# Performance work log

Measured on AMD Instinct MI355X. Metric: run time of the kernel, lower is better.

Reference implementation:

```python
import jax, jax.numpy as jnp
import numpy as np

IN_FEATURES = 4096
OUT_FEATURES = 4096
CODESZ = 8
CODEBOOK_SIZE = 256


def fwht(x):
    """Normalized fast Walsh-Hadamard transform over the last dim (power of 2).
    Equivalent to x @ (H / sqrt(n)); H symmetric so this serves both
    matmul_hadUt and matmul_hadU in the power-of-2 case (had=None, K=1)."""
    orig_shape = x.shape
    n = orig_shape[-1]
    x = x.reshape(-1, n)
    h = 2
    while h <= n:
        x = x.reshape(-1, n // h, 2, h // 2)
        a, b = x[..., 0, :], x[..., 1, :]
        x = jnp.stack([a + b, a - b], axis=-2)
        h *= 2
    x = x.reshape(orig_shape)
    return x * (1.0 / np.sqrt(n)).astype(np.float32)


def setup_inputs() -> dict:
    key = jax.random.key(0)
    k1, k2, k3, k4, k5, k6 = jax.random.split(key, 6)
    x = jax.random.normal(k1, (4, 2048, IN_FEATURES), dtype=jnp.float32)
    Qidxs = jax.random.randint(k2, (OUT_FEATURES, IN_FEATURES // CODESZ), 0, CODEBOOK_SIZE, dtype=jnp.int32)
    grid = jax.random.normal(k3, (CODEBOOK_SIZE, CODESZ), dtype=jnp.float32)
    SU = jax.random.uniform(k4, (IN_FEATURES,), dtype=jnp.float32)
    SV = jax.random.uniform(k5, (OUT_FEATURES,), dtype=jnp.float32)
    bias = jax.random.normal(k6, (OUT_FEATURES,), dtype=jnp.float32)
    return {"x": x, "Qidxs": Qidxs, "grid": grid, "SU": SU, "SV": SV, "bias": bias}


def reference(x, Qidxs, grid, SU, SV, bias):
    lead = x.shape[:-1]
    h = x.reshape(-1, IN_FEATURES)            # [T, in]
    h = h * SU                                 # scale by SU
    h = fwht(h)                                # matmul_hadUt (input rotation)
    # codebook dequant: gather code vectors and form W_hat [out, in]
    W_hat = grid[Qidxs].reshape(OUT_FEATURES, IN_FEATURES)
    y = h @ W_hat.T                            # [T, out]
    y = fwht(y)[:, :OUT_FEATURES]              # matmul_hadU (output rotation)
    y = y * SV
    y = y.reshape(*lead, OUT_FEATURES) + bias
    return y
```

## Files before the change

### kernel.cpp

```cpp
#include <hip/hip_runtime.h>

#define IN_F 4096
#define OUT_F 4096
#define NROWS 8192
#define BK 32
#define NT (IN_F / BK)

typedef __attribute__((ext_vector_type(4))) float f32x4;
typedef __attribute__((ext_vector_type(8))) short bf16x8;
typedef __attribute__((ext_vector_type(8))) unsigned short u16x8;

__device__ __forceinline__ unsigned short f2bf(float f) {
  union { float f; unsigned u; } x; x.f = f;
  unsigned r = x.u + 0x7FFFu + ((x.u >> 16) & 1u);
  return (unsigned short)(r >> 16);
}

__device__ __forceinline__ void gload_lds16(const unsigned short* g, unsigned short* l) {
  __builtin_amdgcn_global_load_lds((__attribute__((address_space(1))) void*)g,
                                   (__attribute__((address_space(3))) void*)l,
                                   16, 0, 0);
}

__device__ __forceinline__ void bfly16(float v[16]) {
#pragma unroll
  for (int s = 1; s < 16; s <<= 1) {
#pragma unroll
    for (int i = 0; i < 16; ++i) {
      if (!(i & s)) { float a = v[i], b = v[i + s]; v[i] = a + b; v[i + s] = a - b; }
    }
  }
}

__global__ __launch_bounds__(256) void dequant_kernel(const int* __restrict__ Q,
                                                      const float* __restrict__ grid,
                                                      unsigned short* __restrict__ Wb) {
  int g = blockIdx.x * 256 + threadIdx.x;
  int idx = Q[g];
  const f32x4* gp = (const f32x4*)(grid + idx * 8);
  f32x4 v0 = gp[0], v1 = gp[1];
  u16x8 o;
  o[0] = f2bf(v0[0]); o[1] = f2bf(v0[1]); o[2] = f2bf(v0[2]); o[3] = f2bf(v0[3]);
  o[4] = f2bf(v1[0]); o[5] = f2bf(v1[1]); o[6] = f2bf(v1[2]); o[7] = f2bf(v1[3]);
  *(u16x8*)(Wb + (size_t)g * 8) = o;
}

__global__ __launch_bounds__(256) void fwht1_kernel(const float* __restrict__ x,
                                                    const float* __restrict__ SU,
                                                    unsigned short* __restrict__ Hb) {
  __shared__ float buf[4096];
  int tid = threadIdx.x;
  size_t rbase = (size_t)blockIdx.x * IN_F;
  const f32x4* x4 = (const f32x4*)(x + rbase);
  const f32x4* su4 = (const f32x4*)SU;
  f32x4* b4 = (f32x4*)buf;
#pragma unroll
  for (int s = 0; s < 4; ++s) {
    int c = tid + 256 * s;
    f32x4 v = x4[c];
    f32x4 u = su4[c];
    v.x *= u.x; v.y *= u.y; v.z *= u.z; v.w *= u.w;
    b4[c] = v;
  }
  __syncthreads();
  float v[16];
  {
#pragma unroll
    for (int j = 0; j < 4; ++j) {
      f32x4 t4 = b4[tid * 4 + j];
      v[j*4+0] = t4.x; v[j*4+1] = t4.y; v[j*4+2] = t4.z; v[j*4+3] = t4.w;
    }
    bfly16(v);
#pragma unroll
    for (int j = 0; j < 4; ++j) {
      f32x4 t4; t4.x = v[j*4+0]; t4.y = v[j*4+1]; t4.z = v[j*4+2]; t4.w = v[j*4+3];
      b4[tid * 4 + j] = t4;
    }
  }
  __syncthreads();
  {
    int lo = tid & 15, hi = tid >> 4;
    int base = lo + (hi << 8);
#pragma unroll
    for (int j = 0; j < 16; ++j) v[j] = buf[base + (j << 4)];
    bfly16(v);
#pragma unroll
    for (int j = 0; j < 16; ++j) buf[base + (j << 4)] = v[j];
  }
  __syncthreads();
  {
#pragma unroll
    for (int j = 0; j < 16; ++j) v[j] = buf[tid + (j << 8)];
    bfly16(v);
#pragma unroll
    for (int j = 0; j < 16; ++j)
      Hb[rbase + tid + (j << 8)] = f2bf(v[j] * 0.015625f);
  }
}

#define MM(i, A, B) acc[i] = __builtin_amdgcn_mfma_f32_16x16x32_bf16(A, B, acc[i], 0, 0, 0)

__global__ __launch_bounds__(512) void gemm256_kernel(const unsigned short* __restrict__ Hb,
                                                      const unsigned short* __restrict__ Wb,
                                                      float* __restrict__ Y) {
  __shared__ unsigned short lds[4][2][256 * BK];
  const int tid = threadIdx.x;
  const int lane = tid & 63;
  const int wid = tid >> 6;
  const int wr = wid >> 2;
  const int wc = wid & 3;
  const int lrow = lane & 15;
  const int kgrp = lane >> 4;

  const int bid = blockIdx.x;
  const int swz = (bid & 7) * 64 + (bid >> 3);
  const int brow = (swz >> 4) << 8;
  const int bcol = (swz & 15) << 8;

  const unsigned short* Ab = Hb + (size_t)brow * IN_F;
  const unsigned short* Bb = Wb + (size_t)bcol * IN_F;

  const int r0 = tid >> 2;
  const int sc = ((tid & 3) ^ (r0 & 3)) << 3;
  const unsigned short* Ag0 = Ab + (size_t)r0 * IN_F + sc;
  const unsigned short* Ag1 = Ab + (size_t)(r0 + 128) * IN_F + sc;
  const unsigned short* Bg0 = Bb + (size_t)r0 * IN_F + sc;
  const unsigned short* Bg1 = Bb + (size_t)(r0 + 128) * IN_F + sc;

#define STAGE_A(t, s) { gload_lds16(Ag0 + (t) * BK, &lds[s][0][tid * 8]); \
                        gload_lds16(Ag1 + (t) * BK, &lds[s][0][(tid + 512) * 8]); }
#define STAGE_B(t, s) { gload_lds16(Bg0 + (t) * BK, &lds[s][1][tid * 8]); \
                        gload_lds16(Bg1 + (t) * BK, &lds[s][1][(tid + 512) * 8]); }

  auto fragLd = [&](const unsigned short* base, int R) -> bf16x8 {
    return *(const bf16x8*)(base + R * BK + ((kgrp ^ (R & 3)) << 3));
  };

  f32x4 acc[32] = {};

  STAGE_A(0, 0); STAGE_B(0, 0);
  STAGE_A(1, 1); STAGE_B(1, 1);
  STAGE_A(2, 2); STAGE_B(2, 2);
  asm volatile("s_waitcnt vmcnt(8)" ::: "memory");
  asm volatile("s_barrier" ::: "memory");

  for (int t = 0; t < NT; ++t) {
    const int s = t & 3;
    const unsigned short* As = &lds[s][0][0];
    const unsigned short* Bs = &lds[s][1][0];
    bf16x8 a0, a1, a2, a3, b0, b1, b2, b3;

    a0 = fragLd(As, wr * 128 +  0 + lrow);
    a1 = fragLd(As, wr * 128 + 16 + lrow);
    a2 = fragLd(As, wr * 128 + 32 + lrow);
    a3 = fragLd(As, wr * 128 + 48 + lrow);
    b0 = fragLd(Bs, wc * 64 +  0 + lrow);
    b1 = fragLd(Bs, wc * 64 + 16 + lrow);
    b2 = fragLd(Bs, wc * 64 + 32 + lrow);
    b3 = fragLd(Bs, wc * 64 + 48 + lrow);
    if (t + 3 < NT) STAGE_A(t + 3, (t + 3) & 3);
    asm volatile("s_barrier" ::: "memory");
    __builtin_amdgcn_s_setprio(1);
    MM( 0, a0, b0); MM( 1, a0, b1); MM( 2, a0, b2); MM( 3, a0, b3);
    MM( 4, a1, b0); MM( 5, a1, b1); MM( 6, a1, b2); MM( 7, a1, b3);
    MM( 8, a2, b0); MM( 9, a2, b1); MM(10, a2, b2); MM(11, a2, b3);
    MM(12, a3, b0); MM(13, a3, b1); MM(14, a3, b2); MM(15, a3, b3);
    __builtin_amdgcn_s_setprio(0);
    asm volatile("s_barrier" ::: "memory");

    a0 = fragLd(As, wr * 128 +  64 + lrow);
    a1 = fragLd(As, wr * 128 +  80 + lrow);
    a2 = fragLd(As, wr * 128 +  96 + lrow);
    a3 = fragLd(As, wr * 128 + 112 + lrow);
    if (t + 3 < NT) STAGE_B(t + 3, (t + 3) & 3);
    asm volatile("s_barrier" ::: "memory");
    __builtin_amdgcn_s_setprio(1);
    MM(16, a0, b0); MM(17, a0, b1); MM(18, a0, b2); MM(19, a0, b3);
    MM(20, a1, b0); MM(21, a1, b1); MM(22, a1, b2); MM(23, a1, b3);
    MM(24, a2, b0); MM(25, a2, b1); MM(26, a2, b2); MM(27, a2, b3);
    MM(28, a3, b0); MM(29, a3, b1); MM(30, a3, b2); MM(31, a3, b3);
    __builtin_amdgcn_s_setprio(0);
    if (t < NT - 3)       { asm volatile("s_waitcnt vmcnt(8)" ::: "memory"); }
    else if (t == NT - 3) { asm volatile("s_waitcnt vmcnt(4)" ::: "memory"); }
    else if (t == NT - 2) { asm volatile("s_waitcnt vmcnt(0)" ::: "memory"); }
    asm volatile("s_barrier" ::: "memory");
  }

#pragma unroll
  for (int mf = 0; mf < 8; ++mf) {
    int grow = brow + wr * 128 + mf * 16 + kgrp * 4;
    float* yp = Y + (size_t)grow * OUT_F + bcol + wc * 64 + lrow;
#pragma unroll
    for (int r = 0; r < 4; ++r)
#pragma unroll
      for (int n = 0; n < 4; ++n)
        yp[(size_t)r * OUT_F + n * 16] = acc[mf * 4 + n][r];
  }
#undef STAGE_A
#undef STAGE_B
}

__global__ __launch_bounds__(256) void fwht2_kernel(float* __restrict__ Y,
                                                    const float* __restrict__ SV,
                                                    const float* __restrict__ bias) {
  __shared__ float buf[4096];
  int tid = threadIdx.x;
  size_t rbase = (size_t)blockIdx.x * OUT_F;
  f32x4* y4 = (f32x4*)(Y + rbase);
  f32x4* b4 = (f32x4*)buf;
#pragma unroll
  for (int s = 0; s < 4; ++s) {
    int c = tid + 256 * s;
    b4[c] = y4[c];
  }
  __syncthreads();
  float v[16];
  {
#pragma unroll
    for (int j = 0; j < 4; ++j) {
      f32x4 t4 = b4[tid * 4 + j];
      v[j*4+0] = t4.x; v[j*4+1] = t4.y; v[j*4+2] = t4.z; v[j*4+3] = t4.w;
    }
    bfly16(v);
#pragma unroll
    for (int j = 0; j < 4; ++j) {
      f32x4 t4; t4.x = v[j*4+0]; t4.y = v[j*4+1]; t4.z = v[j*4+2]; t4.w = v[j*4+3];
      b4[tid * 4 + j] = t4;
    }
  }
  __syncthreads();
  {
    int lo = tid & 15, hi = tid >> 4;
    int base = lo + (hi << 8);
#pragma unroll
    for (int j = 0; j < 16; ++j) v[j] = buf[base + (j << 4)];
    bfly16(v);
#pragma unroll
    for (int j = 0; j < 16; ++j) buf[base + (j << 4)] = v[j];
  }
  __syncthreads();
  {
#pragma unroll
    for (int j = 0; j < 16; ++j) v[j] = buf[tid + (j << 8)];
    bfly16(v);
#pragma unroll
    for (int j = 0; j < 16; ++j) {
      int col = tid + (j << 8);
      Y[rbase + col] = v[j] * 0.015625f * SV[col] + bias[col];
    }
  }
}

extern "C" void kernel_launch(void* const* d_in, const int* in_sizes, int n_in,
                              void* d_out, int out_size, void* d_ws, size_t ws_size,
                              hipStream_t stream) {
  const float* x     = (const float*)d_in[0];
  const int*   Qidxs = (const int*)d_in[1];
  const float* grid  = (const float*)d_in[2];
  const float* SU    = (const float*)d_in[3];
  const float* SV    = (const float*)d_in[4];
  const float* bias  = (const float*)d_in[5];
  float* out = (float*)d_out;

  unsigned short* Wb = (unsigned short*)d_ws;
  unsigned short* Hb = Wb + (size_t)OUT_F * IN_F;

  hipLaunchKernelGGL(dequant_kernel, dim3((OUT_F * (IN_F / 8)) / 256), dim3(256), 0, stream,
                     Qidxs, grid, Wb);
  hipLaunchKernelGGL(fwht1_kernel, dim3(NROWS), dim3(256), 0, stream, x, SU, Hb);
  hipLaunchKernelGGL(gemm256_kernel, dim3((NROWS / 256) * (OUT_F / 256)), dim3(512), 0, stream,
                     Hb, Wb, out);
  hipLaunchKernelGGL(fwht2_kernel, dim3(NROWS), dim3(256), 0, stream, out, SV, bias);
}
```

Measured before the change: 357.2 us.

## Double-buffer LDS fragment registers and change LDS swizzle in GEMM main loop

Restructures the bf16 GEMM main loop to process two K-tiles per iteration with two register fragment sets, so LDS reads for the next tile are issued while MFMAs for the current tile execute. This cuts barriers from three per tile to about one. Global-to-LDS staging now loads the A and B halves together in one STAGE. The LDS XOR swizzle now keys on (row>>1)&3 instead of row&3, to reduce bank conflicts for the 64-byte row stride. The cost is doubled fragment registers, which may raise VGPR pressure and lower occupancy, plus subtler waitcnt bookkeeping around the 4-slot ring.

```diff
diff --git a/kernel.cpp b/kernel.cpp
--- a/kernel.cpp
+++ b/kernel.cpp
@@ -121,69 +121,73 @@
   const unsigned short* Bb = Wb + (size_t)bcol * IN_F;
 
   const int r0 = tid >> 2;
-  const int sc = ((tid & 3) ^ (r0 & 3)) << 3;
+  const int sc = ((tid & 3) ^ ((r0 >> 1) & 3)) << 3;
   const unsigned short* Ag0 = Ab + (size_t)r0 * IN_F + sc;
   const unsigned short* Ag1 = Ab + (size_t)(r0 + 128) * IN_F + sc;
   const unsigned short* Bg0 = Bb + (size_t)r0 * IN_F + sc;
   const unsigned short* Bg1 = Bb + (size_t)(r0 + 128) * IN_F + sc;
 
-#define STAGE_A(t, s) { gload_lds16(Ag0 + (t) * BK, &lds[s][0][tid * 8]); \
-                        gload_lds16(Ag1 + (t) * BK, &lds[s][0][(tid + 512) * 8]); }
-#define STAGE_B(t, s) { gload_lds16(Bg0 + (t) * BK, &lds[s][1][tid * 8]); \
-                        gload_lds16(Bg1 + (t) * BK, &lds[s][1][(tid + 512) * 8]); }
+#define STAGE(t, s) { \
+  gload_lds16(Ag0 + (t) * BK, &lds[s][0][tid * 8]); \
+  gload_lds16(Ag1 + (t) * BK, &lds[s][0][(tid + 512) * 8]); \
+  gload_lds16(Bg0 + (t) * BK, &lds[s][1][tid * 8]); \
+  gload_lds16(Bg1 + (t) * BK, &lds[s][1][(tid + 512) * 8]); }
 
   auto fragLd = [&](const unsigned short* base, int R) -> bf16x8 {
-    return *(const bf16x8*)(base + R * BK + ((kgrp ^ (R & 3)) << 3));
+    return *(const bf16x8*)(base + R * BK + ((kgrp ^ ((R >> 1) & 3)) << 3));
   };
 
+  const int ar = wr * 128 + lrow;
+  const int br = wc * 64 + lrow;
+
+#define READ_SET(aS, bS, slot) { \
+  const unsigned short* As_ = &lds[slot][0][0]; \
+  const unsigned short* Bs_ = &lds[slot][1][0]; \
+  aS[0] = fragLd(As_, ar +   0); aS[1] = fragLd(As_, ar +  16); \
+  aS[2] = fragLd(As_, ar +  32); aS[3] = fragLd(As_, ar +  48); \
+  aS[4] = fragLd(As_, ar +  64); aS[5] = fragLd(As_, ar +  80); \
+  aS[6] = fragLd(As_, ar +  96); aS[7] = fragLd(As_, ar + 112); \
+  bS[0] = fragLd(Bs_, br +   0); bS[1] = fragLd(Bs_, br +  16); \
+  bS[2] = fragLd(Bs_, br +  32); bS[3] = fragLd(Bs_, br +  48); }
+
+#define MFMA_SET(aS, bS) { \
+  __builtin_amdgcn_s_setprio(1); \
+  MM( 0, aS[0], bS[0]); MM( 1, aS[0], bS[1]); MM( 2, aS[0], bS[2]); MM( 3, aS[0], bS[3]); \
+  MM( 4, aS[1], bS[0]); MM( 5, aS[1], bS[1]); MM( 6, aS[1], bS[2]); MM( 7, aS[1], bS[3]); \
+  MM( 8, aS[2], bS[0]); MM( 9, aS[2], bS[1]); MM(10, aS[2], bS[2]); MM(11, aS[2], bS[3]); \
+  MM(12, aS[3], bS[0]); MM(13, aS[3], bS[1]); MM(14, aS[3], bS[2]); MM(15, aS[3], bS[3]); \
+  MM(16, aS[4], bS[0]); MM(17, aS[4], bS[1]); MM(18, aS[4], bS[2]); MM(19, aS[4], bS[3]); \
+  MM(20, aS[5], bS[0]); MM(21, aS[5], bS[1]); MM(22, aS[5], bS[2]); MM(23, aS[5], bS[3]); \
+  MM(24, aS[6], bS[0]); MM(25, aS[6], bS[1]); MM(26, aS[6], bS[2]); MM(27, aS[6], bS[3]); \
+  MM(28, aS[7], bS[0]); MM(29, aS[7], bS[1]); MM(30, aS[7], bS[2]); MM(31, aS[7], bS[3]); \
+  __builtin_amdgcn_s_setprio(0); }
+
   f32x4 acc[32] = {};
-
-  STAGE_A(0, 0); STAGE_B(0, 0);
-  STAGE_A(1, 1); STAGE_B(1, 1);
-  STAGE_A(2, 2); STAGE_B(2, 2);
-  asm volatile("s_waitcnt vmcnt(8)" ::: "memory");
+  bf16x8 aA[8], bA[4], aB[8], bB[4];
+
+  STAGE(0, 0); STAGE(1, 1); STAGE(2, 2);
+  asm volatile("s_waitcnt vmcnt(4)" ::: "memory");
   asm volatile("s_barrier" ::: "memory");
-
-  for (int t = 0; t < NT; ++t) {
-    const int s = t & 3;
-    const unsigned short* As = &lds[s][0][0];
-    const unsigned short* Bs = &lds[s][1][0];
-    bf16x8 a0, a1, a2, a3, b0, b1, b2, b3;
-
-    a0 = fragLd(As, wr * 128 +  0 + lrow);
-    a1 = fragLd(As, wr * 128 + 16 + lrow);
-    a2 = fragLd(As, wr * 128 + 32 + lrow);
-    a3 = fragLd(As, wr * 128 + 48 + lrow);
-    b0 = fragLd(Bs, wc * 64 +  0 + lrow);
-    b1 = fragLd(Bs, wc * 64 + 16 + lrow);
-    b2 = fragLd(Bs, wc * 64 + 32 + lrow);
-    b3 = fragLd(Bs, wc * 64 + 48 + lrow);
-    if (t + 3 < NT) STAGE_A(t + 3, (t + 3) & 3);
-    asm volatile("s_barrier" ::: "memory");
-    __builtin_amdgcn_s_setprio(1);
-    MM( 0, a0, b0); MM( 1, a0, b1); MM( 2, a0, b2); MM( 3, a0, b3);
-    MM( 4, a1, b0); MM( 5, a1, b1); MM( 6, a1, b2); MM( 7, a1, b3);
-    MM( 8, a2, b0); MM( 9, a2, b1); MM(10, a2, b2); MM(11, a2, b3);
-    MM(12, a3, b0); MM(13, a3, b1); MM(14, a3, b2); MM(15, a3, b3);
-    __builtin_amdgcn_s_setprio(0);
-    asm volatile("s_barrier" ::: "memory");
-
-    a0 = fragLd(As, wr * 128 +  64 + lrow);
-    a1 = fragLd(As, wr * 128 +  80 + lrow);
-    a2 = fragLd(As, wr * 128 +  96 + lrow);
-    a3 = fragLd(As, wr * 128 + 112 + lrow);
-    if (t + 3 < NT) STAGE_B(t + 3, (t + 3) & 3);
-    asm volatile("s_barrier" ::: "memory");
-    __builtin_amdgcn_s_setprio(1);
-    MM(16, a0, b0); MM(17, a0, b1); MM(18, a0, b2); MM(19, a0, b3);
-    MM(20, a1, b0); MM(21, a1, b1); MM(22, a1, b2); MM(23, a1, b3);
-    MM(24, a2, b0); MM(25, a2, b1); MM(26, a2, b2); MM(27, a2, b3);
-    MM(28, a3, b0); MM(29, a3, b1); MM(30, a3, b2); MM(31, a3, b3);
-    __builtin_amdgcn_s_setprio(0);
-    if (t < NT - 3)       { asm volatile("s_waitcnt vmcnt(8)" ::: "memory"); }
-    else if (t == NT - 3) { asm volatile("s_waitcnt vmcnt(4)" ::: "memory"); }
-    else if (t == NT - 2) { asm volatile("s_waitcnt vmcnt(0)" ::: "memory"); }
-    asm volatile("s_barrier" ::: "memory");
+  READ_SET(aA, bA, 0);
+
+  for (int t = 0; t < NT; t += 2) {
+    if (t) {
+      if (t + 2 < NT) { asm volatile("s_waitcnt vmcnt(4)" ::: "memory"); }
+      else            { asm volatile("s_waitcnt vmcnt(0)" ::: "memory"); }
+      asm volatile("s_barrier" ::: "memory");
+    }
+    if (t + 3 < NT) STAGE(t + 3, (t + 3) & 3);
+    READ_SET(aB, bB, (t + 1) & 3);
+    MFMA_SET(aA, bA);
+
+    if (t + 2 < NT) {
+      if (t + 4 < NT) { asm volatile("s_waitcnt vmcnt(4)" ::: "memory"); }
+      else            { asm volatile("s_waitcnt vmcnt(0)" ::: "memory"); }
+      asm volatile("s_barrier" ::: "memory");
+      if (t + 4 < NT) STAGE(t + 4, (t + 4) & 3);
+      READ_SET(aA, bA, (t + 2) & 3);
+    }
+    MFMA_SET(aB, bB);
   }
 
 #pragma unroll
@@ -196,8 +200,9 @@
       for (int n = 0; n < 4; ++n)
         yp[(size_t)r * OUT_F + n * 16] = acc[mf * 4 + n][r];
   }
-#undef STAGE_A
-#undef STAGE_B
+#undef STAGE
+#undef READ_SET
+#undef MFMA_SET
 }
 
 __global__ __launch_bounds__(256) void fwht2_kernel(float* __restrict__ Y,
```

New measurement: 357.6 us. About the same (+0.1%).
